# Performance work log

Hardware: AMD Instinct MI355X
Metric: run time of the kernel (lower is better)

The kernel has to match this reference:

```python
import jax, jax.numpy as jnp
import numpy as np
from jax import lax

B = 4            # batch (number of point clouds)
N_PER = 8192     # points per cloud
STRIDE = 4
M_PER = N_PER // STRIDE   # sampled points per cloud
K = 16           # nsample
C_IN = 64
C_OUT = 128
EPS = 1e-5


def fps(pts, m):
    """Furthest point sampling on (n,3), returns m int32 indices, starts at 0."""
    n = pts.shape[0]

    def step(carry, _):
        dist, last = carry
        d = jnp.sum((pts - pts[last]) ** 2, axis=-1)
        dist = jnp.minimum(dist, d)
        nxt = jnp.argmax(dist).astype(jnp.int32)
        return (dist, nxt), nxt

    init = (jnp.full((n,), 1e10, dtype=pts.dtype), jnp.int32(0))
    _, idxs = lax.scan(step, init, None, length=m - 1)
    return jnp.concatenate([jnp.zeros((1,), jnp.int32), idxs])


def knn_idx(pts, queries, k):
    """Indices of k nearest points for each query. pts (n,3), queries (m,3)."""
    d2 = (jnp.sum(queries * queries, -1)[:, None]
          + jnp.sum(pts * pts, -1)[None, :]
          - 2.0 * (queries @ pts.T))            # (m, n)
    _, idx = lax.top_k(-d2, k)                   # smallest distances
    return idx


def setup_inputs() -> dict:
    key = jax.random.key(0)
    k1, k2, k3 = jax.random.split(key, 3)
    point = jax.random.normal(k1, (B * N_PER, 3), dtype=jnp.float32) * 5.0
    feat = jax.random.normal(k2, (B * N_PER, C_IN), dtype=jnp.float32)
    row_splits = (jnp.arange(B + 1, dtype=jnp.int64) * N_PER)
    W = jax.random.normal(k3, (C_OUT, 3 + C_IN), dtype=jnp.float32) * 0.05
    gamma = jnp.ones((C_OUT,), dtype=jnp.float32)
    beta = jnp.zeros((C_OUT,), dtype=jnp.float32)
    return {"point": point, "feat": feat, "row_splits": row_splits,
            "W": W, "gamma": gamma, "beta": beta}


def reference(point, feat, row_splits, W, gamma, beta):
    pb = point.reshape(B, N_PER, 3)
    fb = feat.reshape(B, N_PER, C_IN)

    # --- furthest point sampling (non-differentiable index op) ---
    sidx = jax.vmap(lambda p: fps(p, M_PER))(lax.stop_gradient(pb))   # (B, M)
    new_p = jnp.take_along_axis(pb, sidx[..., None], axis=1)          # (B, M, 3)

    # --- batched KNN (indices only, like knn_search) ---
    nidx = jax.vmap(knn_idx, in_axes=(0, 0, None))(
        lax.stop_gradient(pb), lax.stop_gradient(new_p), K)           # (B, M, K)

    # --- queryandgroup: gather neighbors, relative xyz, concat feat ---
    gxyz = jax.vmap(lambda p, i: p[i])(pb, nidx) - new_p[:, :, None]  # (B, M, K, 3)
    gfeat = jax.vmap(lambda f, i: f[i])(fb, nidx)                     # (B, M, K, C_IN)
    g = jnp.concatenate([gxyz, gfeat], axis=-1).reshape(B * M_PER, K, 3 + C_IN)

    # --- linear (no bias) -> BN (batch stats over points & neighbors) -> ReLU ---
    y = jnp.einsum('mkc,oc->mko', g, W)                               # (m, K, C_OUT)
    mean = jnp.mean(y, axis=(0, 1))
    var = jnp.mean(jnp.square(y - mean), axis=(0, 1))                 # biased var
    y = (y - mean) * (gamma * lax.rsqrt(var + EPS)) + beta
    y = jax.nn.relu(y)

    # --- maxpool over neighbors ---
    out_feat = jnp.max(y, axis=1)                                     # (m, C_OUT)

    new_point = new_p.reshape(B * M_PER, 3)
    new_row_splits = jnp.arange(B + 1, dtype=jnp.int64) * M_PER
    return new_point, out_feat, new_row_splits
```

## Files before the change

kernel.cpp:

```cpp
#include <hip/hip_runtime.h>

#define NB 4
#define NPER 8192
#define MPER 2048
#define KNN 16
#define CIN 64
#define CO 128
#define MTOT (NB*MPER)

typedef unsigned long long u64;
typedef unsigned int u32;

__device__ __forceinline__ float med3f(float a, float b, float c) {
    return __builtin_amdgcn_fmed3f(a, b, c);
}

__global__ void k_init(float* __restrict__ stats, float* __restrict__ rs) {
    int t = threadIdx.x;
    if (t < 256) stats[t] = 0.f;
    if (t < 5) rs[t] = (float)(t * MPER);
}

#define DPPSTEP(key, CTRL, RM) do {                                                   \
    unsigned lo_ = (unsigned)(key), hi_ = (unsigned)((key) >> 32);                    \
    unsigned nlo = (unsigned)__builtin_amdgcn_update_dpp((int)lo_, (int)lo_, CTRL, RM, 0xf, false); \
    unsigned nhi = (unsigned)__builtin_amdgcn_update_dpp((int)hi_, (int)hi_, CTRL, RM, 0xf, false); \
    unsigned long long ok_ = ((unsigned long long)nhi << 32) | nlo;                   \
    if (ok_ > (key)) (key) = ok_;                                                     \
} while (0)

#define DPP6(key) do { \
    DPPSTEP(key, 0xB1,  0xF); \
    DPPSTEP(key, 0x4E,  0xF); \
    DPPSTEP(key, 0x141, 0xF); \
    DPPSTEP(key, 0x140, 0xF); \
    DPPSTEP(key, 0x142, 0xA); \
    DPPSTEP(key, 0x143, 0xC); \
} while (0)

__launch_bounds__(512, 2)
__global__ void k_fps(const float* __restrict__ pts, float* __restrict__ out_np,
                      float4* __restrict__ qpts) {
    #pragma clang fp contract(off)
    __shared__ float4 spt[NPER];
    __shared__ u64 red[2][8];
    const int b = blockIdx.x;
    const int t = threadIdx.x;
    const float4* pb4 = (const float4*)(pts + (size_t)b * NPER * 3);

    float f[48];
    #pragma unroll
    for (int j = 0; j < 12; ++j) {
        float4 v = pb4[t * 12 + j];
        f[j*4+0] = v.x; f[j*4+1] = v.y; f[j*4+2] = v.z; f[j*4+3] = v.w;
    }
    float px[16], py[16], pz[16], dd[16];
    #pragma unroll
    for (int s = 0; s < 16; ++s) {
        px[s] = f[3*s]; py[s] = f[3*s+1]; pz[s] = f[3*s+2];
        dd[s] = 1e10f;
        spt[t * 16 + s] = make_float4(px[s], py[s], pz[s], 0.f);
    }
    if (t == 0) {
        size_t row = (size_t)b * MPER;
        out_np[row*3+0] = px[0]; out_np[row*3+1] = py[0]; out_np[row*3+2] = pz[0];
        qpts[row] = make_float4(px[0], py[0], pz[0], 0.f);
    }
    __syncthreads();

    float4 c0 = spt[0];
    float cx = c0.x, cy = c0.y, cz = c0.z;
    const int ibase = t * 16;

    for (int i = 1; i < MPER; ++i) {
        float bv = -1.f; int bs = 0;
        #pragma unroll
        for (int s = 0; s < 16; ++s) {
            float dx = px[s] - cx, dy = py[s] - cy, dz = pz[s] - cz;
            float t0 = dx * dx, t1 = dy * dy, t2 = dz * dz;
            float d = (t0 + t1) + t2;
            float nd = fminf(dd[s], d);
            dd[s] = nd;
            bool bet = nd > bv;
            bv = bet ? nd : bv;
            bs = bet ? s : bs;
        }
        u64 key = ((u64)__float_as_uint(bv) << 32) | (u32)~(u32)(ibase + bs);

        DPP6(key);

        if ((t & 63) == 63) red[i & 1][t >> 6] = key;
        __syncthreads();

        const int p = i & 1;
        u64 k0 = red[p][0], k1 = red[p][1], k2 = red[p][2], k3 = red[p][3];
        u64 k4 = red[p][4], k5 = red[p][5], k6 = red[p][6], k7 = red[p][7];
        u64 a0 = k0 > k1 ? k0 : k1, a1 = k2 > k3 ? k2 : k3;
        u64 a2 = k4 > k5 ? k4 : k5, a3 = k6 > k7 ? k6 : k7;
        u64 b0 = a0 > a1 ? a0 : a1, b1 = a2 > a3 ? a2 : a3;
        u64 kbest = b0 > b1 ? b0 : b1;
        const int i2 = (int)(~(u32)kbest & 0x1FFFu);

        float4 c = spt[i2];
        cx = c.x; cy = c.y; cz = c.z;

        if (t == 0) {
            size_t row = (size_t)b * MPER + i;
            out_np[row*3+0] = cx; out_np[row*3+1] = cy; out_np[row*3+2] = cz;
            qpts[row] = make_float4(cx, cy, cz, 0.f);
        }
    }
}

#define CCAP 28
__launch_bounds__(256, 1)
__global__ void k_knn(const float* __restrict__ pts, const float4* __restrict__ qpts,
                      int* __restrict__ nidx) {
    #pragma clang fp contract(off)
    __shared__ float4 sp[2][4][514];
    __shared__ float  ndl[256][16];
    __shared__ u32    candl[256][CCAP];
    __shared__ int    ccnt[256], ccless[256];
    __shared__ float  taub[64];

    const int t = threadIdx.x;
    const int qloc = t >> 2, sub = t & 3;
    const int q = blockIdx.x * 64 + qloc;
    const int b = q >> 11;
    const float4 qp = qpts[q];
    const float qq = (qp.x * qp.x + qp.y * qp.y) + qp.z * qp.z;
    const float* pb = pts + (size_t)b * NPER * 3;
    const int wq = t >> 6, wl = t & 63;

    float4 L[6];
    #define LOADC(c) do { const float4* src_ = (const float4*)(pb + (size_t)(c) * 2048 * 3); \
        _Pragma("unroll") for (int u_ = 0; u_ < 6; ++u_) L[u_] = src_[t * 6 + u_]; } while (0)
    #define WRITEC(pbuf) do { \
        float fl_[24]; \
        _Pragma("unroll") for (int u_ = 0; u_ < 6; ++u_) { \
            fl_[u_*4+0]=L[u_].x; fl_[u_*4+1]=L[u_].y; fl_[u_*4+2]=L[u_].z; fl_[u_*4+3]=L[u_].w; } \
        _Pragma("unroll") for (int r_ = 0; r_ < 8; ++r_) { \
            float x_=fl_[3*r_], y_=fl_[3*r_+1], z_=fl_[3*r_+2]; \
            float pp_=(x_*x_ + y_*y_) + z_*z_; \
            sp[pbuf][wq][wl*8 + r_] = make_float4(x_,y_,z_,pp_); } } while (0)

    float nd[16];
    #pragma unroll
    for (int j = 0; j < 16; ++j) nd[j] = 1e30f;

    LOADC(0); WRITEC(0); LOADC(1);
    __syncthreads();
    for (int c = 0; c < 4; ++c) {
        const int pbuf = c & 1;
        #pragma unroll 4
        for (int j = 0; j < 512; ++j) {
            float4 p = sp[pbuf][sub][j];
            float dot = (qp.x * p.x + qp.y * p.y) + qp.z * p.z;
            float d = (qq + p.w) - 2.f * dot;
            if (d < nd[15]) {
                #pragma unroll
                for (int u = 15; u >= 1; --u) nd[u] = med3f(d, nd[u-1], nd[u]);
                nd[0] = fminf(nd[0], d);
            }
        }
        __syncthreads();
        if (c < 3) {
            WRITEC((c + 1) & 1);
            if (c < 2) LOADC(c + 2);
            __syncthreads();
        }
    }
    #pragma unroll
    for (int j = 0; j < 16; ++j) ndl[t][j] = nd[j];
    __syncthreads();

    if (sub == 0) {
        int p0=0,p1=0,p2=0,p3=0;
        float c0=ndl[t][0], c1=ndl[t+1][0], c2=ndl[t+2][0], c3=ndl[t+3][0];
        float tau = 0.f;
        for (int it = 0; it < 16; ++it) {
            if (c0 <= c1 && c0 <= c2 && c0 <= c3) { tau=c0; ++p0; c0 = (p0<16)?ndl[t][p0]:1e30f; }
            else if (c1 <= c2 && c1 <= c3)        { tau=c1; ++p1; c1 = (p1<16)?ndl[t+1][p1]:1e30f; }
            else if (c2 <= c3)                    { tau=c2; ++p2; c2 = (p2<16)?ndl[t+2][p2]:1e30f; }
            else                                  { tau=c3; ++p3; c3 = (p3<16)?ndl[t+3][p3]:1e30f; }
        }
        taub[qloc] = tau;
    }
    __syncthreads();
    const float tau = taub[qloc];

    int cnt = 0, cless = 0;
    LOADC(0); WRITEC(0); LOADC(1);
    __syncthreads();
    for (int c = 0; c < 4; ++c) {
        const int pbuf = c & 1;
        for (int j = 0; j < 512; ++j) {
            float4 p = sp[pbuf][sub][j];
            float dot = (qp.x * p.x + qp.y * p.y) + qp.z * p.z;
            float d = (qq + p.w) - 2.f * dot;
            if (d <= tau && cnt < CCAP) {
                bool eq = !(d < tau);
                candl[t][cnt++] = (u32)(c * 2048 + sub * 512 + j) | (eq ? 0x80000000u : 0u);
                if (!eq) cless++;
            }
        }
        __syncthreads();
        if (c < 3) {
            WRITEC((c + 1) & 1);
            if (c < 2) LOADC(c + 2);
            __syncthreads();
        }
    }
    ccnt[t] = cnt; ccless[t] = cless;
    __syncthreads();

    if (sub == 0) {
        int n0=ccnt[t], n1=ccnt[t+1], n2=ccnt[t+2], n3=ccnt[t+3];
        int quota = 16 - (ccless[t]+ccless[t+1]+ccless[t+2]+ccless[t+3]);
        int p0=0,p1=0,p2=0,p3=0, kept=0, eq_used=0;
        u32 h0 = n0 ? candl[t][0]   : 0xFFFFFFFFu;
        u32 h1 = n1 ? candl[t+1][0] : 0xFFFFFFFFu;
        u32 h2 = n2 ? candl[t+2][0] : 0xFFFFFFFFu;
        u32 h3 = n3 ? candl[t+3][0] : 0xFFFFFFFFu;
        size_t obase = (size_t)q * KNN;
        for (int g = 0; g < 4*CCAP && kept < 16; ++g) {
            u32 m0 = h0 & 0x7fffffffu, m1 = h1 & 0x7fffffffu;
            u32 m2 = h2 & 0x7fffffffu, m3 = h3 & 0x7fffffffu;
            u32 v;
            if (m0 <= m1 && m0 <= m2 && m0 <= m3) { v=h0; ++p0; h0 = (p0<n0)?candl[t][p0]:0xFFFFFFFFu; }
            else if (m1 <= m2 && m1 <= m3)        { v=h1; ++p1; h1 = (p1<n1)?candl[t+1][p1]:0xFFFFFFFFu; }
            else if (m2 <= m3)                    { v=h2; ++p2; h2 = (p2<n2)?candl[t+2][p2]:0xFFFFFFFFu; }
            else                                  { v=h3; ++p3; h3 = (p3<n3)?candl[t+3][p3]:0xFFFFFFFFu; }
            if (v == 0xFFFFFFFFu) break;
            bool eq = (v >> 31) != 0;
            bool take = !eq || (eq_used < quota);
            if (take) {
                if (eq) ++eq_used;
                nidx[obase + kept] = b * NPER + (int)(v & 0x7fffffffu);
                ++kept;
            }
        }
    }
    #undef LOADC
    #undef WRITEC
}

__launch_bounds__(128, 4)
__global__ void k_stats(const float* __restrict__ pts, const float* __restrict__ feat,
                        const float* __restrict__ W, const int* __restrict__ nidx,
                        const float4* __restrict__ qpts, float* __restrict__ ymax,
                        float* __restrict__ ymin, float* __restrict__ stats) {
    __shared__ float4 g4[KNN][17];
    const int t = threadIdx.x;
    float w[68];
    const float* wr = W + t * 67;
    #pragma unroll
    for (int c = 0; c < 64; ++c) w[c] = wr[3 + c];
    w[64] = wr[0]; w[65] = wr[1]; w[66] = wr[2]; w[67] = 0.f;

    float s_sum = 0.f, s_sq = 0.f;
    const int k0 = t >> 3, p8 = t & 7;
    for (int mi = 0; mi < 8; ++mi) {
        const int m0 = blockIdx.x * 8 + mi;
        {
            int nid = nidx[(size_t)m0 * KNN + k0];
            const float4* fr = (const float4*)(feat + (size_t)nid * CIN);
            g4[k0][p8*2]   = fr[p8*2];
            g4[k0][p8*2+1] = fr[p8*2+1];
        }
        if (t < 16) {
            int nid = nidx[(size_t)m0 * KNN + t];
            float4 qp = qpts[m0];
            float x = pts[(size_t)nid*3], y = pts[(size_t)nid*3+1], z = pts[(size_t)nid*3+2];
            g4[t][16] = make_float4(x - qp.x, y - qp.y, z - qp.z, 0.f);
        }
        __syncthreads();
        float vmax = -1e30f, vmin = 1e30f;
        #pragma unroll 1
        for (int k = 0; k < KNN; ++k) {
            float y0 = 0.f, y1 = 0.f, y2 = 0.f, y3 = 0.f;
            #pragma unroll
            for (int c4 = 0; c4 < 17; ++c4) {
                float4 gv = g4[k][c4];
                y0 = fmaf(gv.x, w[c4*4+0], y0);
                y1 = fmaf(gv.y, w[c4*4+1], y1);
                y2 = fmaf(gv.z, w[c4*4+2], y2);
                y3 = fmaf(gv.w, w[c4*4+3], y3);
            }
            float y = (y0 + y1) + (y2 + y3);
            vmax = fmaxf(vmax, y); vmin = fminf(vmin, y);
            s_sum += y; s_sq = fmaf(y, y, s_sq);
        }
        ymax[(size_t)m0 * CO + t] = vmax;
        ymin[(size_t)m0 * CO + t] = vmin;
        __syncthreads();
    }
    atomicAdd(stats + t, s_sum);
    atomicAdd(stats + CO + t, s_sq);
}

__global__ void k_final(const float* __restrict__ stats, const float* __restrict__ gamma,
                        const float* __restrict__ beta, float* __restrict__ sb) {
    int o = threadIdx.x;
    const float inv = 1.f / (float)(MTOT * KNN);
    float mean = stats[o] * inv;
    float var = stats[CO + o] * inv - mean * mean;
    var = fmaxf(var, 0.f);
    float s = gamma[o] * rsqrtf(var + 1e-5f);
    sb[o] = s;
    sb[CO + o] = beta[o] - mean * s;
}

__global__ void k_out(const float* __restrict__ ymax, const float* __restrict__ ymin,
                      const float* __restrict__ sb, float* __restrict__ out_feat) {
    int tid = blockIdx.x * 256 + threadIdx.x;
    int o = tid & (CO - 1);
    float s = sb[o], bb = sb[CO + o];
    float yv = (s >= 0.f) ? ymax[tid] : ymin[tid];
    out_feat[tid] = fmaxf(fmaf(s, yv, bb), 0.f);
}

extern "C" void kernel_launch(void* const* d_in, const int* in_sizes, int n_in,
                              void* d_out, int out_size, void* d_ws, size_t ws_size,
                              hipStream_t stream) {
    const float* pts   = (const float*)d_in[0];
    const float* feat  = (const float*)d_in[1];
    const float* W     = (const float*)d_in[3];
    const float* gamma = (const float*)d_in[4];
    const float* beta  = (const float*)d_in[5];
    float* out = (float*)d_out;
    char* ws = (char*)d_ws;

    float4* qpts = (float4*)(ws);
    int*    nidx = (int*)(ws + 131072);
    float*  stats = (float*)(ws + 655360);
    float*  sb    = (float*)(ws + 656384);
    float*  ymax  = (float*)(ws + 657408);
    float*  ymin  = (float*)(ws + 657408 + 4194304);

    float* out_np   = out;
    float* out_feat = out + 24576;
    float* out_rs   = out + 24576 + 1048576;

    hipLaunchKernelGGL(k_init,  dim3(1), dim3(256), 0, stream, stats, out_rs);
    hipLaunchKernelGGL(k_fps,   dim3(NB), dim3(512), 0, stream, pts, out_np, qpts);
    hipLaunchKernelGGL(k_knn,   dim3(MTOT / 64), dim3(256), 0, stream, pts, qpts, nidx);
    hipLaunchKernelGGL(k_stats, dim3(MTOT / 8), dim3(128), 0, stream,
                       pts, feat, W, nidx, qpts, ymax, ymin, stats);
    hipLaunchKernelGGL(k_final, dim3(1), dim3(128), 0, stream, stats, gamma, beta, sb);
    hipLaunchKernelGGL(k_out,   dim3(MTOT * CO / 256), dim3(256), 0, stream,
                       ymax, ymin, sb, out_feat);
}
```

Measured before the change: 2.458 ms.

## Morton-sort FPS points per thread and skip distance updates via bbox bounds

Before furthest point sampling starts, the points are quantized and sorted by Morton code with a shared-memory bitonic sort, so each thread owns a spatially compact group of 16 points with its own bounding box. On each iteration a thread computes a lower bound on the distance from the new centroid to its box. If that bound exceeds its current best distance it skips the 16-point min-distance update and reuses its cached key. The key encoding now carries the original index for tie-breaking and the sorted slot for the lookup. This adds a one-time sort and extra registers (launch bounds drop to one block per CU) in exchange for skipping most per-iteration arithmetic; the 1.001 slack on the skip test adds a small exactness risk.

Result: slower. 4.271 ms (+73.8%).

```diff
diff --git a/kernel.cpp b/kernel.cpp
--- a/kernel.cpp
+++ b/kernel.cpp
@@ -38,15 +38,22 @@
     DPPSTEP(key, 0x143, 0xC); \
 } while (0)
 
-__launch_bounds__(512, 2)
+__launch_bounds__(512, 1)
 __global__ void k_fps(const float* __restrict__ pts, float* __restrict__ out_np,
                       float4* __restrict__ qpts) {
     #pragma clang fp contract(off)
-    __shared__ float4 spt[NPER];
+    __shared__ __align__(16) char smraw[NPER * 16];
     __shared__ u64 red[2][8];
+    __shared__ float gb[8][6];
+    __shared__ int slot0sh;
+    u32*    sdu = (u32*)smraw;
+    float4* spt = (float4*)smraw;
+
     const int b = blockIdx.x;
     const int t = threadIdx.x;
-    const float4* pb4 = (const float4*)(pts + (size_t)b * NPER * 3);
+    const int ibase = t * 16;
+    const float* pb = pts + (size_t)b * NPER * 3;
+    const float4* pb4 = (const float4*)pb;
 
     float f[48];
     #pragma unroll
@@ -55,41 +62,124 @@
         f[j*4+0] = v.x; f[j*4+1] = v.y; f[j*4+2] = v.z; f[j*4+3] = v.w;
     }
     float px[16], py[16], pz[16], dd[16];
+    int or16[16];
+    #pragma unroll
+    for (int s = 0; s < 16; ++s) { px[s] = f[3*s]; py[s] = f[3*s+1]; pz[s] = f[3*s+2]; }
+
+    float mnx=1e30f,mny=1e30f,mnz=1e30f,mxx=-1e30f,mxy=-1e30f,mxz=-1e30f;
     #pragma unroll
     for (int s = 0; s < 16; ++s) {
-        px[s] = f[3*s]; py[s] = f[3*s+1]; pz[s] = f[3*s+2];
-        dd[s] = 1e10f;
-        spt[t * 16 + s] = make_float4(px[s], py[s], pz[s], 0.f);
-    }
+        mnx=fminf(mnx,px[s]); mxx=fmaxf(mxx,px[s]);
+        mny=fminf(mny,py[s]); mxy=fmaxf(mxy,py[s]);
+        mnz=fminf(mnz,pz[s]); mxz=fmaxf(mxz,pz[s]);
+    }
+    #pragma unroll
+    for (int off=1; off<64; off<<=1) {
+        mnx=fminf(mnx,__shfl_xor(mnx,off)); mxx=fmaxf(mxx,__shfl_xor(mxx,off));
+        mny=fminf(mny,__shfl_xor(mny,off)); mxy=fmaxf(mxy,__shfl_xor(mxy,off));
+        mnz=fminf(mnz,__shfl_xor(mnz,off)); mxz=fmaxf(mxz,__shfl_xor(mxz,off));
+    }
+    if ((t&63)==0) {
+        int w = t>>6;
+        gb[w][0]=mnx; gb[w][1]=mny; gb[w][2]=mnz; gb[w][3]=mxx; gb[w][4]=mxy; gb[w][5]=mxz;
+    }
+    __syncthreads();
+    mnx=1e30f; mny=1e30f; mnz=1e30f; mxx=-1e30f; mxy=-1e30f; mxz=-1e30f;
+    #pragma unroll
+    for (int w = 0; w < 8; ++w) {
+        mnx=fminf(mnx,gb[w][0]); mny=fminf(mny,gb[w][1]); mnz=fminf(mnz,gb[w][2]);
+        mxx=fmaxf(mxx,gb[w][3]); mxy=fmaxf(mxy,gb[w][4]); mxz=fmaxf(mxz,gb[w][5]);
+    }
+    float scx = 63.0f / fmaxf(mxx-mnx, 1e-20f);
+    float scy = 63.0f / fmaxf(mxy-mny, 1e-20f);
+    float scz = 63.0f / fmaxf(mxz-mnz, 1e-20f);
+
+    #pragma unroll
+    for (int s = 0; s < 16; ++s) {
+        u32 qx = (u32)min(63, max(0, (int)((px[s]-mnx)*scx)));
+        u32 qy = (u32)min(63, max(0, (int)((py[s]-mny)*scy)));
+        u32 qz = (u32)min(63, max(0, (int)((pz[s]-mnz)*scz)));
+        u32 mx_=qx, my_=qy, mz_=qz;
+        #define P1B2(v) do { v=(v|(v<<8))&0x0300F00Fu; v=(v|(v<<4))&0x030C30C3u; v=(v|(v<<2))&0x09249249u; } while(0)
+        P1B2(mx_); P1B2(my_); P1B2(mz_);
+        u32 m = (mx_<<2)|(my_<<1)|mz_;
+        sdu[ibase + s] = (m << 13) | (u32)(ibase + s);
+    }
+    __syncthreads();
+
+    for (u32 kk2 = 2; kk2 <= NPER; kk2 <<= 1) {
+        for (u32 j = kk2 >> 1; j > 0; j >>= 1) {
+            for (int ii = t; ii < NPER; ii += 512) {
+                int l = ii ^ (int)j;
+                if (l > ii) {
+                    u32 a = sdu[ii], bb = sdu[l];
+                    bool asc = ((ii & (int)kk2) == 0);
+                    if ((a > bb) == asc) { sdu[ii] = bb; sdu[l] = a; }
+                }
+            }
+            __syncthreads();
+        }
+    }
+
+    u32 kreg[16];
+    #pragma unroll
+    for (int s = 0; s < 16; ++s) kreg[s] = sdu[ibase + s];
+    __syncthreads();
+
+    float bx0=1e30f,by0=1e30f,bz0=1e30f,bx1=-1e30f,by1=-1e30f,bz1=-1e30f;
+    #pragma unroll
+    for (int s = 0; s < 16; ++s) {
+        int orig = (int)(kreg[s] & 0x1FFFu);
+        float x = pb[orig*3], y = pb[orig*3+1], z = pb[orig*3+2];
+        px[s]=x; py[s]=y; pz[s]=z; or16[s]=orig; dd[s]=1e10f;
+        spt[ibase + s] = make_float4(x, y, z, 0.f);
+        if (orig == 0) slot0sh = ibase + s;
+        bx0=fminf(bx0,x); bx1=fmaxf(bx1,x);
+        by0=fminf(by0,y); by1=fmaxf(by1,y);
+        bz0=fminf(bz0,z); bz1=fmaxf(bz1,z);
+    }
+    __syncthreads();
+
+    float4 c0 = spt[slot0sh];
+    float cx = c0.x, cy = c0.y, cz = c0.z;
     if (t == 0) {
         size_t row = (size_t)b * MPER;
-        out_np[row*3+0] = px[0]; out_np[row*3+1] = py[0]; out_np[row*3+2] = pz[0];
-        qpts[row] = make_float4(px[0], py[0], pz[0], 0.f);
-    }
-    __syncthreads();
-
-    float4 c0 = spt[0];
-    float cx = c0.x, cy = c0.y, cz = c0.z;
-    const int ibase = t * 16;
+        out_np[row*3+0]=cx; out_np[row*3+1]=cy; out_np[row*3+2]=cz;
+        qpts[row] = make_float4(cx, cy, cz, 0.f);
+    }
+
+    float bv = 1e10f;
+    u64 key = 0;
 
     for (int i = 1; i < MPER; ++i) {
-        float bv = -1.f; int bs = 0;
-        #pragma unroll
-        for (int s = 0; s < 16; ++s) {
-            float dx = px[s] - cx, dy = py[s] - cy, dz = pz[s] - cz;
-            float t0 = dx * dx, t1 = dy * dy, t2 = dz * dz;
-            float d = (t0 + t1) + t2;
-            float nd = fminf(dd[s], d);
-            dd[s] = nd;
-            bool bet = nd > bv;
-            bv = bet ? nd : bv;
-            bs = bet ? s : bs;
-        }
-        u64 key = ((u64)__float_as_uint(bv) << 32) | (u32)~(u32)(ibase + bs);
-
-        DPP6(key);
-
-        if ((t & 63) == 63) red[i & 1][t >> 6] = key;
+        float ex = fmaxf(fmaxf(bx0 - cx, cx - bx1), 0.f);
+        float ey = fmaxf(fmaxf(by0 - cy, cy - by1), 0.f);
+        float ez = fmaxf(fmaxf(bz0 - cz, cz - bz1), 0.f);
+        float lb = fmaf(ex, ex, fmaf(ey, ey, ez * ez));
+        if (!(lb > bv * 1.001f)) {
+            float nbv = -1.f; int nbo = 0x7FFFFFFF; int nbs = 0;
+            #pragma unroll
+            for (int s = 0; s < 16; ++s) {
+                float dx = px[s]-cx, dy = py[s]-cy, dz = pz[s]-cz;
+                float t0 = dx*dx, t1 = dy*dy, t2 = dz*dz;
+                float d = (t0 + t1) + t2;
+                float nd = fminf(dd[s], d);
+                dd[s] = nd;
+                bool bet = (nd > nbv) || ((nd == nbv) && (or16[s] < nbo));
+                nbv = bet ? nd : nbv;
+                nbo = bet ? or16[s] : nbo;
+                nbs = bet ? s : nbs;
+            }
+            bv = nbv;
+            key = ((u64)__float_as_uint(nbv) << 26)
+                | ((u64)((~(u32)nbo) & 0x1FFFu) << 13)
+                | (u32)(ibase + nbs);
+        }
+
+        u64 rk = key;
+        DPP6(rk);
+
+        if ((t & 63) == 63) red[i & 1][t >> 6] = rk;
         __syncthreads();
 
         const int p = i & 1;
@@ -99,9 +189,9 @@
         u64 a2 = k4 > k5 ? k4 : k5, a3 = k6 > k7 ? k6 : k7;
         u64 b0 = a0 > a1 ? a0 : a1, b1 = a2 > a3 ? a2 : a3;
         u64 kbest = b0 > b1 ? b0 : b1;
-        const int i2 = (int)(~(u32)kbest & 0x1FFFu);
-
-        float4 c = spt[i2];
+        const int wslot = (int)(kbest & 0x1FFFu);
+
+        float4 c = spt[wslot];
         cx = c.x; cy = c.y; cz = c.z;
 
         if (t == 0) {
```

## Fuse FPS and KNN into one persistent kernel with progress-flag overlap

Applied to the files above, without the earlier changes.

Merges the furthest-point-sampling and KNN kernels into a single launch. The first 4 blocks run FPS (now 256 threads holding 32 points each) and publish progress every 64 samples through an atomic counter. The remaining blocks spin-wait on that counter and then run KNN for their query chunk, so KNN overlaps with the serial FPS tail. It also folds the BN finalize kernel into the output kernel. The risks are deadlock if KNN blocks occupy all CUs before the FPS blocks are scheduled, and a slower FPS inner loop now that each thread handles twice as many points.

After: 2.355 ms. 4.2% less time.

```diff
diff --git a/kernel.cpp b/kernel.cpp
--- a/kernel.cpp
+++ b/kernel.cpp
@@ -7,6 +7,7 @@
 #define CIN 64
 #define CO 128
 #define MTOT (NB*MPER)
+#define CCAP 28
 
 typedef unsigned long long u64;
 typedef unsigned int u32;
@@ -15,9 +16,11 @@
     return __builtin_amdgcn_fmed3f(a, b, c);
 }
 
-__global__ void k_init(float* __restrict__ stats, float* __restrict__ rs) {
+__global__ void k_init(float* __restrict__ stats, float* __restrict__ rs,
+                       u32* __restrict__ prog) {
     int t = threadIdx.x;
     if (t < 256) stats[t] = 0.f;
+    if (t < 4) prog[t] = 0u;
     if (t < 5) rs[t] = (float)(t * MPER);
 }
 
@@ -38,211 +41,228 @@
     DPPSTEP(key, 0x143, 0xC); \
 } while (0)
 
-__launch_bounds__(512, 2)
-__global__ void k_fps(const float* __restrict__ pts, float* __restrict__ out_np,
-                      float4* __restrict__ qpts) {
+struct FpsSM {
+    float4 spt[NPER];
+    u64 red[2][4];
+};
+struct KnnSM {
+    float4 sp[2][4][514];
+    float  ndl[256][16];
+    u32    candl[256][CCAP];
+    int    ccnt[256], ccless[256];
+    float  taub[64];
+};
+#define SMBYTES (sizeof(FpsSM) > sizeof(KnnSM) ? sizeof(FpsSM) : sizeof(KnnSM))
+
+__launch_bounds__(256, 1)
+__global__ void k_mega(const float* __restrict__ pts, float* __restrict__ out_np,
+                       float4* __restrict__ qpts, u32* __restrict__ prog,
+                       int* __restrict__ nidx) {
     #pragma clang fp contract(off)
-    __shared__ float4 spt[NPER];
-    __shared__ u64 red[2][8];
-    const int b = blockIdx.x;
+    __shared__ __align__(16) char SMRAW[SMBYTES];
     const int t = threadIdx.x;
-    const float4* pb4 = (const float4*)(pts + (size_t)b * NPER * 3);
-
-    float f[48];
-    #pragma unroll
-    for (int j = 0; j < 12; ++j) {
-        float4 v = pb4[t * 12 + j];
-        f[j*4+0] = v.x; f[j*4+1] = v.y; f[j*4+2] = v.z; f[j*4+3] = v.w;
+
+    if (blockIdx.x < NB) {
+        FpsSM& sm = *(FpsSM*)SMRAW;
+        const int b = blockIdx.x;
+        const float4* pb4 = (const float4*)(pts + (size_t)b * NPER * 3);
+
+        float f[96];
+        #pragma unroll
+        for (int j = 0; j < 24; ++j) {
+            float4 v = pb4[t * 24 + j];
+            f[j*4+0] = v.x; f[j*4+1] = v.y; f[j*4+2] = v.z; f[j*4+3] = v.w;
+        }
+        float px[32], py[32], pz[32], dd[32];
+        #pragma unroll
+        for (int s = 0; s < 32; ++s) {
+            px[s] = f[3*s]; py[s] = f[3*s+1]; pz[s] = f[3*s+2];
+            dd[s] = 1e10f;
+            sm.spt[t * 32 + s] = make_float4(px[s], py[s], pz[s], 0.f);
+        }
+        if (t == 0) {
+            size_t row = (size_t)b * MPER;
+            out_np[row*3+0] = px[0]; out_np[row*3+1] = py[0]; out_np[row*3+2] = pz[0];
+            qpts[row] = make_float4(px[0], py[0], pz[0], 0.f);
+        }
+        __syncthreads();
+
+        float4 c0 = sm.spt[0];
+        float cx = c0.x, cy = c0.y, cz = c0.z;
+        const int lane = t & 63, wv = t >> 6;
+        const int ibase = t * 32;
+
+        for (int i = 1; i < MPER; ++i) {
+            float bv = -1.f; int bs = 0;
+            #pragma unroll
+            for (int s = 0; s < 32; ++s) {
+                float dx = px[s] - cx, dy = py[s] - cy, dz = pz[s] - cz;
+                float t0 = dx * dx, t1 = dy * dy, t2 = dz * dz;
+                float d = (t0 + t1) + t2;
+                float nd = fminf(dd[s], d);
+                dd[s] = nd;
+                bool bet = nd > bv;
+                bv = bet ? nd : bv;
+                bs = bet ? s : bs;
+            }
+            u64 key = ((u64)__float_as_uint(bv) << 32) | (u32)~(u32)(ibase + bs);
+
+            DPP6(key);
+
+            if (lane == 63) sm.red[i & 1][wv] = key;
+            __syncthreads();
+
+            const int p = i & 1;
+            u64 k0 = sm.red[p][0], k1 = sm.red[p][1], k2 = sm.red[p][2], k3 = sm.red[p][3];
+            u64 ka = k0 > k1 ? k0 : k1;
+            u64 kb = k2 > k3 ? k2 : k3;
+            u64 kbest = ka > kb ? ka : kb;
+            const int i2 = (int)(~(u32)kbest) & 0x1FFF;
+
+            float4 c = sm.spt[i2];
+            cx = c.x; cy = c.y; cz = c.z;
+
+            if (t == 0) {
+                size_t row = (size_t)b * MPER + i;
+                out_np[row*3+0] = cx; out_np[row*3+1] = cy; out_np[row*3+2] = cz;
+                qpts[row] = make_float4(cx, cy, cz, 0.f);
+                if ((i & 63) == 63) {
+                    __threadfence();
+                    __hip_atomic_store(prog + b, (u32)(i + 1),
+                                       __ATOMIC_RELEASE, __HIP_MEMORY_SCOPE_AGENT);
+                }
+            }
+        }
+    } else {
+        KnnSM& sm = *(KnnSM*)SMRAW;
+        const int kb = blockIdx.x - NB;
+        const int q0 = kb * 64;
+        const int b = q0 >> 11;
+        const u32 need = (u32)(((q0 + 63) & (MPER - 1)) + 1);
+
+        while (__hip_atomic_load(prog + b, __ATOMIC_RELAXED, __HIP_MEMORY_SCOPE_AGENT) < need)
+            __builtin_amdgcn_s_sleep(8);
+        __threadfence();
+
+        const int qloc = t >> 2, sub = t & 3;
+        const int q = q0 + qloc;
+        const float4 qp = qpts[q];
+        const float qq = (qp.x * qp.x + qp.y * qp.y) + qp.z * qp.z;
+        const float* pb = pts + (size_t)b * NPER * 3;
+        const int wq = t >> 6, wl = t & 63;
+
+        float4 L[6];
+        #define LOADC(c) do { const float4* src_ = (const float4*)(pb + (size_t)(c) * 2048 * 3); \
+            _Pragma("unroll") for (int u_ = 0; u_ < 6; ++u_) L[u_] = src_[t * 6 + u_]; } while (0)
+        #define WRITEC(pbuf) do { \
+            float fl_[24]; \
+            _Pragma("unroll") for (int u_ = 0; u_ < 6; ++u_) { \
+                fl_[u_*4+0]=L[u_].x; fl_[u_*4+1]=L[u_].y; fl_[u_*4+2]=L[u_].z; fl_[u_*4+3]=L[u_].w; } \
+            _Pragma("unroll") for (int r_ = 0; r_ < 8; ++r_) { \
+                float x_=fl_[3*r_], y_=fl_[3*r_+1], z_=fl_[3*r_+2]; \
+                float pp_=(x_*x_ + y_*y_) + z_*z_; \
+                sm.sp[pbuf][wq][wl*8 + r_] = make_float4(x_,y_,z_,pp_); } } while (0)
+
+        float nd[16];
+        #pragma unroll
+        for (int j = 0; j < 16; ++j) nd[j] = 1e30f;
+
+        LOADC(0); WRITEC(0); LOADC(1);
+        __syncthreads();
+        for (int c = 0; c < 4; ++c) {
+            const int pbuf = c & 1;
+            #pragma unroll 4
+            for (int j = 0; j < 512; ++j) {
+                float4 p = sm.sp[pbuf][sub][j];
+                float dot = (qp.x * p.x + qp.y * p.y) + qp.z * p.z;
+                float d = (qq + p.w) - 2.f * dot;
+                if (d < nd[15]) {
+                    #pragma unroll
+                    for (int u = 15; u >= 1; --u) nd[u] = med3f(d, nd[u-1], nd[u]);
+                    nd[0] = fminf(nd[0], d);
+                }
+            }
+            __syncthreads();
+            if (c < 3) {
+                WRITEC((c + 1) & 1);
+                if (c < 2) LOADC(c + 2);
+                __syncthreads();
+            }
+        }
+        #pragma unroll
+        for (int j = 0; j < 16; ++j) sm.ndl[t][j] = nd[j];
+        __syncthreads();
+
+        if (sub == 0) {
+            int p0=0,p1=0,p2=0,p3=0;
+            float c0=sm.ndl[t][0], c1=sm.ndl[t+1][0], c2=sm.ndl[t+2][0], c3=sm.ndl[t+3][0];
+            float tau = 0.f;
+            for (int it = 0; it < 16; ++it) {
+                if (c0 <= c1 && c0 <= c2 && c0 <= c3) { tau=c0; ++p0; c0 = (p0<16)?sm.ndl[t][p0]:1e30f; }
+                else if (c1 <= c2 && c1 <= c3)        { tau=c1; ++p1; c1 = (p1<16)?sm.ndl[t+1][p1]:1e30f; }
+                else if (c2 <= c3)                    { tau=c2; ++p2; c2 = (p2<16)?sm.ndl[t+2][p2]:1e30f; }
+                else                                  { tau=c3; ++p3; c3 = (p3<16)?sm.ndl[t+3][p3]:1e30f; }
+            }
+            sm.taub[qloc] = tau;
+        }
+        __syncthreads();
+        const float tau = sm.taub[qloc];
+
+        int cnt = 0, cless = 0;
+        LOADC(0); WRITEC(0); LOADC(1);
+        __syncthreads();
+        for (int c = 0; c < 4; ++c) {
+            const int pbuf = c & 1;
+            for (int j = 0; j < 512; ++j) {
+                float4 p = sm.sp[pbuf][sub][j];
+                float dot = (qp.x * p.x + qp.y * p.y) + qp.z * p.z;
+                float d = (qq + p.w) - 2.f * dot;
+                if (d <= tau && cnt < CCAP) {
+                    bool eq = !(d < tau);
+                    sm.candl[t][cnt++] = (u32)(c * 2048 + sub * 512 + j) | (eq ? 0x80000000u : 0u);
+                    if (!eq) cless++;
+                }
+            }
+            __syncthreads();
+            if (c < 3) {
+                WRITEC((c + 1) & 1);
+                if (c < 2) LOADC(c + 2);
+                __syncthreads();
+            }
+        }
+        sm.ccnt[t] = cnt; sm.ccless[t] = cless;
+        __syncthreads();
+
+        if (sub == 0) {
+            int n0=sm.ccnt[t], n1=sm.ccnt[t+1], n2=sm.ccnt[t+2], n3=sm.ccnt[t+3];
+            int quota = 16 - (sm.ccless[t]+sm.ccless[t+1]+sm.ccless[t+2]+sm.ccless[t+3]);
+            int p0=0,p1=0,p2=0,p3=0, kept=0, eq_used=0;
+            u32 h0 = n0 ? sm.candl[t][0]   : 0xFFFFFFFFu;
+            u32 h1 = n1 ? sm.candl[t+1][0] : 0xFFFFFFFFu;
+            u32 h2 = n2 ? sm.candl[t+2][0] : 0xFFFFFFFFu;
+            u32 h3 = n3 ? sm.candl[t+3][0] : 0xFFFFFFFFu;
+            size_t obase = (size_t)q * KNN;
+            for (int g = 0; g < 4*CCAP && kept < 16; ++g) {
+                u32 m0 = h0 & 0x7fffffffu, m1 = h1 & 0x7fffffffu;
+                u32 m2 = h2 & 0x7fffffffu, m3 = h3 & 0x7fffffffu;
+                u32 v;
+                if (m0 <= m1 && m0 <= m2 && m0 <= m3) { v=h0; ++p0; h0 = (p0<n0)?sm.candl[t][p0]:0xFFFFFFFFu; }
+                else if (m1 <= m2 && m1 <= m3)        { v=h1; ++p1; h1 = (p1<n1)?sm.candl[t+1][p1]:0xFFFFFFFFu; }
+                else if (m2 <= m3)                    { v=h2; ++p2; h2 = (p2<n2)?sm.candl[t+2][p2]:0xFFFFFFFFu; }
+                else                                  { v=h3; ++p3; h3 = (p3<n3)?sm.candl[t+3][p3]:0xFFFFFFFFu; }
+                if (v == 0xFFFFFFFFu) break;
+                bool eq = (v >> 31) != 0;
+                bool take = !eq || (eq_used < quota);
+                if (take) {
+                    if (eq) ++eq_used;
+                    nidx[obase + kept] = b * NPER + (int)(v & 0x7fffffffu);
+                    ++kept;
+                }
+            }
+        }
+        #undef LOADC
+        #undef WRITEC
     }
-    float px[16], py[16], pz[16], dd[16];
-    #pragma unroll
-    for (int s = 0; s < 16; ++s) {
-        px[s] = f[3*s]; py[s] = f[3*s+1]; pz[s] = f[3*s+2];
-        dd[s] = 1e10f;
-        spt[t * 16 + s] = make_float4(px[s], py[s], pz[s], 0.f);
-    }
-    if (t == 0) {
-        size_t row = (size_t)b * MPER;
-        out_np[row*3+0] = px[0]; out_np[row*3+1] = py[0]; out_np[row*3+2] = pz[0];
-        qpts[row] = make_float4(px[0], py[0], pz[0], 0.f);
-    }
-    __syncthreads();
-
-    float4 c0 = spt[0];
-    float cx = c0.x, cy = c0.y, cz = c0.z;
-    const int ibase = t * 16;
-
-    for (int i = 1; i < MPER; ++i) {
-        float bv = -1.f; int bs = 0;
-        #pragma unroll
-        for (int s = 0; s < 16; ++s) {
-            float dx = px[s] - cx, dy = py[s] - cy, dz = pz[s] - cz;
-            float t0 = dx * dx, t1 = dy * dy, t2 = dz * dz;
-            float d = (t0 + t1) + t2;
-            float nd = fminf(dd[s], d);
-            dd[s] = nd;
-            bool bet = nd > bv;
-            bv = bet ? nd : bv;
-            bs = bet ? s : bs;
-        }
-        u64 key = ((u64)__float_as_uint(bv) << 32) | (u32)~(u32)(ibase + bs);
-
-        DPP6(key);
-
-        if ((t & 63) == 63) red[i & 1][t >> 6] = key;
-        __syncthreads();
-
-        const int p = i & 1;
-        u64 k0 = red[p][0], k1 = red[p][1], k2 = red[p][2], k3 = red[p][3];
-        u64 k4 = red[p][4], k5 = red[p][5], k6 = red[p][6], k7 = red[p][7];
-        u64 a0 = k0 > k1 ? k0 : k1, a1 = k2 > k3 ? k2 : k3;
-        u64 a2 = k4 > k5 ? k4 : k5, a3 = k6 > k7 ? k6 : k7;
-        u64 b0 = a0 > a1 ? a0 : a1, b1 = a2 > a3 ? a2 : a3;
-        u64 kbest = b0 > b1 ? b0 : b1;
-        const int i2 = (int)(~(u32)kbest & 0x1FFFu);
-
-        float4 c = spt[i2];
-        cx = c.x; cy = c.y; cz = c.z;
-
-        if (t == 0) {
-            size_t row = (size_t)b * MPER + i;
-            out_np[row*3+0] = cx; out_np[row*3+1] = cy; out_np[row*3+2] = cz;
-            qpts[row] = make_float4(cx, cy, cz, 0.f);
-        }
-    }
-}
-
-#define CCAP 28
-__launch_bounds__(256, 1)
-__global__ void k_knn(const float* __restrict__ pts, const float4* __restrict__ qpts,
-                      int* __restrict__ nidx) {
-    #pragma clang fp contract(off)
-    __shared__ float4 sp[2][4][514];
-    __shared__ float  ndl[256][16];
-    __shared__ u32    candl[256][CCAP];
-    __shared__ int    ccnt[256], ccless[256];
-    __shared__ float  taub[64];
-
-    const int t = threadIdx.x;
-    const int qloc = t >> 2, sub = t & 3;
-    const int q = blockIdx.x * 64 + qloc;
-    const int b = q >> 11;
-    const float4 qp = qpts[q];
-    const float qq = (qp.x * qp.x + qp.y * qp.y) + qp.z * qp.z;
-    const float* pb = pts + (size_t)b * NPER * 3;
-    const int wq = t >> 6, wl = t & 63;
-
-    float4 L[6];
-    #define LOADC(c) do { const float4* src_ = (const float4*)(pb + (size_t)(c) * 2048 * 3); \
-        _Pragma("unroll") for (int u_ = 0; u_ < 6; ++u_) L[u_] = src_[t * 6 + u_]; } while (0)
-    #define WRITEC(pbuf) do { \
-        float fl_[24]; \
-        _Pragma("unroll") for (int u_ = 0; u_ < 6; ++u_) { \
-            fl_[u_*4+0]=L[u_].x; fl_[u_*4+1]=L[u_].y; fl_[u_*4+2]=L[u_].z; fl_[u_*4+3]=L[u_].w; } \
-        _Pragma("unroll") for (int r_ = 0; r_ < 8; ++r_) { \
-            float x_=fl_[3*r_], y_=fl_[3*r_+1], z_=fl_[3*r_+2]; \
-            float pp_=(x_*x_ + y_*y_) + z_*z_; \
-            sp[pbuf][wq][wl*8 + r_] = make_float4(x_,y_,z_,pp_); } } while (0)
-
-    float nd[16];
-    #pragma unroll
-    for (int j = 0; j < 16; ++j) nd[j] = 1e30f;
-
-    LOADC(0); WRITEC(0); LOADC(1);
-    __syncthreads();
-    for (int c = 0; c < 4; ++c) {
-        const int pbuf = c & 1;
-        #pragma unroll 4
-        for (int j = 0; j < 512; ++j) {
-            float4 p = sp[pbuf][sub][j];
-            float dot = (qp.x * p.x + qp.y * p.y) + qp.z * p.z;
-            float d = (qq + p.w) - 2.f * dot;
-            if (d < nd[15]) {
-                #pragma unroll
-                for (int u = 15; u >= 1; --u) nd[u] = med3f(d, nd[u-1], nd[u]);
-                nd[0] = fminf(nd[0], d);
-            }
-        }
-        __syncthreads();
-        if (c < 3) {
-            WRITEC((c + 1) & 1);
-            if (c < 2) LOADC(c + 2);
-            __syncthreads();
-        }
-    }
-    #pragma unroll
-    for (int j = 0; j < 16; ++j) ndl[t][j] = nd[j];
-    __syncthreads();
-
-    if (sub == 0) {
-        int p0=0,p1=0,p2=0,p3=0;
-        float c0=ndl[t][0], c1=ndl[t+1][0], c2=ndl[t+2][0], c3=ndl[t+3][0];
-        float tau = 0.f;
-        for (int it = 0; it < 16; ++it) {
-            if (c0 <= c1 && c0 <= c2 && c0 <= c3) { tau=c0; ++p0; c0 = (p0<16)?ndl[t][p0]:1e30f; }
-            else if (c1 <= c2 && c1 <= c3)        { tau=c1; ++p1; c1 = (p1<16)?ndl[t+1][p1]:1e30f; }
-            else if (c2 <= c3)                    { tau=c2; ++p2; c2 = (p2<16)?ndl[t+2][p2]:1e30f; }
-            else                                  { tau=c3; ++p3; c3 = (p3<16)?ndl[t+3][p3]:1e30f; }
-        }
-        taub[qloc] = tau;
-    }
-    __syncthreads();
-    const float tau = taub[qloc];
-
-    int cnt = 0, cless = 0;
-    LOADC(0); WRITEC(0); LOADC(1);
-    __syncthreads();
-    for (int c = 0; c < 4; ++c) {
-        const int pbuf = c & 1;
-        for (int j = 0; j < 512; ++j) {
-            float4 p = sp[pbuf][sub][j];
-            float dot = (qp.x * p.x + qp.y * p.y) + qp.z * p.z;
-            float d = (qq + p.w) - 2.f * dot;
-            if (d <= tau && cnt < CCAP) {
-                bool eq = !(d < tau);
-                candl[t][cnt++] = (u32)(c * 2048 + sub * 512 + j) | (eq ? 0x80000000u : 0u);
-                if (!eq) cless++;
-            }
-        }
-        __syncthreads();
-        if (c < 3) {
-            WRITEC((c + 1) & 1);
-            if (c < 2) LOADC(c + 2);
-            __syncthreads();
-        }
-    }
-    ccnt[t] = cnt; ccless[t] = cless;
-    __syncthreads();
-
-    if (sub == 0) {
-        int n0=ccnt[t], n1=ccnt[t+1], n2=ccnt[t+2], n3=ccnt[t+3];
-        int quota = 16 - (ccless[t]+ccless[t+1]+ccless[t+2]+ccless[t+3]);
-        int p0=0,p1=0,p2=0,p3=0, kept=0, eq_used=0;
-        u32 h0 = n0 ? candl[t][0]   : 0xFFFFFFFFu;
-        u32 h1 = n1 ? candl[t+1][0] : 0xFFFFFFFFu;
-        u32 h2 = n2 ? candl[t+2][0] : 0xFFFFFFFFu;
-        u32 h3 = n3 ? candl[t+3][0] : 0xFFFFFFFFu;
-        size_t obase = (size_t)q * KNN;
-        for (int g = 0; g < 4*CCAP && kept < 16; ++g) {
-            u32 m0 = h0 & 0x7fffffffu, m1 = h1 & 0x7fffffffu;
-            u32 m2 = h2 & 0x7fffffffu, m3 = h3 & 0x7fffffffu;
-            u32 v;
-            if (m0 <= m1 && m0 <= m2 && m0 <= m3) { v=h0; ++p0; h0 = (p0<n0)?candl[t][p0]:0xFFFFFFFFu; }
-            else if (m1 <= m2 && m1 <= m3)        { v=h1; ++p1; h1 = (p1<n1)?candl[t+1][p1]:0xFFFFFFFFu; }
-            else if (m2 <= m3)                    { v=h2; ++p2; h2 = (p2<n2)?candl[t+2][p2]:0xFFFFFFFFu; }
-            else                                  { v=h3; ++p3; h3 = (p3<n3)?candl[t+3][p3]:0xFFFFFFFFu; }
-            if (v == 0xFFFFFFFFu) break;
-            bool eq = (v >> 31) != 0;
-            bool take = !eq || (eq_used < quota);
-            if (take) {
-                if (eq) ++eq_used;
-                nidx[obase + kept] = b * NPER + (int)(v & 0x7fffffffu);
-                ++kept;
-            }
-        }
-    }
-    #undef LOADC
-    #undef WRITEC
 }
 
 __launch_bounds__(128, 4)
@@ -299,23 +319,17 @@
     atomicAdd(stats + CO + t, s_sq);
 }
 
-__global__ void k_final(const float* __restrict__ stats, const float* __restrict__ gamma,
-                        const float* __restrict__ beta, float* __restrict__ sb) {
-    int o = threadIdx.x;
+__global__ void k_out(const float* __restrict__ ymax, const float* __restrict__ ymin,
+                      const float* __restrict__ stats, const float* __restrict__ gamma,
+                      const float* __restrict__ beta, float* __restrict__ out_feat) {
+    int tid = blockIdx.x * 256 + threadIdx.x;
+    int o = tid & (CO - 1);
     const float inv = 1.f / (float)(MTOT * KNN);
     float mean = stats[o] * inv;
     float var = stats[CO + o] * inv - mean * mean;
     var = fmaxf(var, 0.f);
     float s = gamma[o] * rsqrtf(var + 1e-5f);
-    sb[o] = s;
-    sb[CO + o] = beta[o] - mean * s;
-}
-
-__global__ void k_out(const float* __restrict__ ymax, const float* __restrict__ ymin,
-                      const float* __restrict__ sb, float* __restrict__ out_feat) {
-    int tid = blockIdx.x * 256 + threadIdx.x;
-    int o = tid & (CO - 1);
-    float s = sb[o], bb = sb[CO + o];
+    float bb = beta[o] - mean * s;
     float yv = (s >= 0.f) ? ymax[tid] : ymin[tid];
     out_feat[tid] = fmaxf(fmaf(s, yv, bb), 0.f);
 }
@@ -334,7 +348,7 @@
     float4* qpts = (float4*)(ws);
     int*    nidx = (int*)(ws + 131072);
     float*  stats = (float*)(ws + 655360);
-    float*  sb    = (float*)(ws + 656384);
+    u32*    prog  = (u32*)(ws + 656384);
     float*  ymax  = (float*)(ws + 657408);
     float*  ymin  = (float*)(ws + 657408 + 4194304);
 
@@ -342,12 +356,11 @@
     float* out_feat = out + 24576;
     float* out_rs   = out + 24576 + 1048576;
 
-    hipLaunchKernelGGL(k_init,  dim3(1), dim3(256), 0, stream, stats, out_rs);
-    hipLaunchKernelGGL(k_fps,   dim3(NB), dim3(512), 0, stream, pts, out_np, qpts);
-    hipLaunchKernelGGL(k_knn,   dim3(MTOT / 64), dim3(256), 0, stream, pts, qpts, nidx);
+    hipLaunchKernelGGL(k_init,  dim3(1), dim3(256), 0, stream, stats, out_rs, prog);
+    hipLaunchKernelGGL(k_mega,  dim3(NB + MTOT / 64), dim3(256), 0, stream,
+                       pts, out_np, qpts, prog, nidx);
     hipLaunchKernelGGL(k_stats, dim3(MTOT / 8), dim3(128), 0, stream,
                        pts, feat, W, nidx, qpts, ymax, ymin, stats);
-    hipLaunchKernelGGL(k_final, dim3(1), dim3(128), 0, stream, stats, gamma, beta, sb);
     hipLaunchKernelGGL(k_out,   dim3(MTOT * CO / 256), dim3(256), 0, stream,
-                       ymax, ymin, sb, out_feat);
-}
+                       ymax, ymin, stats, gamma, beta, out_feat);
+}
```
